# Kernel tuning notes

Measured on AMD Instinct MI355X. Metric: run time of the kernel, lower is better.

Reference implementation:

```python
import jax, jax.numpy as jnp
import numpy as np

D_IN = 1024
D_OUT = 1024
NUM_HEADS = 16
HEAD_DIM = D_OUT // NUM_HEADS


def setup_inputs() -> dict:
    key = jax.random.key(0)
    k_x, k_qkv, k_pw, k_pb = jax.random.split(key, 4)
    x = jax.random.normal(k_x, (2, 2048, D_IN), dtype=jnp.float32)
    # torch nn.Linear(d_in, 3*d_out, bias=False): weight [3*d_out, d_in]
    w_qkv = jax.random.normal(k_qkv, (3 * D_OUT, D_IN), dtype=jnp.float32) * (1.0 / np.sqrt(D_IN))
    # proj: nn.Linear(d_out, d_out) with bias
    w_proj = jax.random.normal(k_pw, (D_OUT, D_OUT), dtype=jnp.float32) * (1.0 / np.sqrt(D_OUT))
    b_proj = jax.random.normal(k_pb, (D_OUT,), dtype=jnp.float32) * 0.01
    return {"x": x, "w_qkv": w_qkv, "w_proj": w_proj, "b_proj": b_proj}


def reference(x, w_qkv, w_proj, b_proj):
    B, S, _ = x.shape
    # fused QKV projection: [B,S,3*D_OUT]
    qkv = jnp.einsum('bsd,ed->bse', x, w_qkv)
    qkv = qkv.reshape(B, S, 3, NUM_HEADS, HEAD_DIM)
    q, k, v = jnp.moveaxis(qkv, 2, 0)  # each [B,S,H,Dh]
    scale = 1.0 / jnp.sqrt(jnp.asarray(HEAD_DIM, dtype=x.dtype))
    # scores [B,H,S,S]
    scores = jnp.einsum('bqhd,bkhd->bhqk', q, k) * scale
    causal = jnp.tril(jnp.ones((S, S), dtype=bool))
    scores = jnp.where(causal, scores, jnp.asarray(-jnp.inf, dtype=scores.dtype))
    attn = jax.nn.softmax(scores, axis=-1)
    ctx = jnp.einsum('bhqk,bkhd->bqhd', attn, v)  # [B,S,H,Dh]
    ctx = ctx.reshape(B, S, D_OUT)
    return jnp.einsum('bsd,ed->bse', ctx, w_proj) + b_proj
```

## Files before the change

kernel.cpp:

```cpp
#include <hip/hip_runtime.h>
#include <hip/hip_bf16.h>
#include <cstdint>

#define B_SZ   2
#define S_LEN  2048
#define NH     16
#define NT     32
#define LDA    72

using f32x4 = __attribute__((ext_vector_type(4))) float;
typedef __bf16 bf16x8 __attribute__((ext_vector_type(8)));
typedef __bf16 bf16x4 __attribute__((ext_vector_type(4)));

__device__ inline float bf2f(unsigned short u) {
    union { unsigned int i; float f; } v; v.i = ((unsigned int)u) << 16; return v.f;
}
__device__ inline unsigned short f2bf(float f) {
    union { float f; unsigned int i; } v; v.f = f;
    unsigned int r = v.i + 0x7fff + ((v.i >> 16) & 1);
    return (unsigned short)(r >> 16);
}
__device__ inline f32x4 mfma16(bf16x8 a, bf16x8 b, f32x4 c) {
    return __builtin_amdgcn_mfma_f32_16x16x32_bf16(a, b, c, 0, 0, 0);
}
__device__ inline unsigned pack_bf16x2(float lo, float hi) {
    float2 f2; f2.x = lo; f2.y = hi;
    __hip_bfloat162 bb = __float22bfloat162_rn(f2);
    union { __hip_bfloat162 b; unsigned u; } cv; cv.b = bb;
    return cv.u;
}
__device__ inline void ldsbar() {
    __builtin_amdgcn_sched_barrier(0);
    asm volatile("s_waitcnt lgkmcnt(0)" ::: "memory");
    __builtin_amdgcn_s_barrier();
    __builtin_amdgcn_sched_barrier(0);
}
__device__ inline void stC(float* C, size_t idx, float v)  { C[idx] = v; }
__device__ inline void stC(__bf16* C, size_t idx, float v) { ((unsigned short*)C)[idx] = f2bf(v); }

__global__ __launch_bounds__(256) void f2b2_kernel(
    const float* __restrict__ a, int na4, __bf16* __restrict__ outa,
    const float* __restrict__ b, int nb4, __bf16* __restrict__ outb)
{
    int i = blockIdx.x * blockDim.x + threadIdx.x;
    const float* src; __bf16* dst; int idx;
    if (i < na4)           { src = a; dst = outa; idx = i; }
    else if (i < na4 + nb4){ src = b; dst = outb; idx = i - na4; }
    else return;
    float4 v = ((const float4*)src)[idx];
    ushort4 o;
    o.x = f2bf(v.x); o.y = f2bf(v.y); o.z = f2bf(v.z); o.w = f2bf(v.w);
    ((ushort4*)dst)[idx] = o;
}

__global__ __launch_bounds__(256) void f2b_kernel(
    const float* __restrict__ in, __bf16* __restrict__ out, int n4)
{
    int i = blockIdx.x * blockDim.x + threadIdx.x;
    if (i < n4) {
        float4 v = ((const float4*)in)[i];
        ushort4 o;
        o.x = f2bf(v.x); o.y = f2bf(v.y); o.z = f2bf(v.z); o.w = f2bf(v.w);
        ((ushort4*)out)[i] = o;
    }
}

template <typename TO, int HAS_BIAS>
__global__ __launch_bounds__(256) void gemm128(
    const __bf16* __restrict__ A, const __bf16* __restrict__ W,
    const float* __restrict__ bias, TO* __restrict__ C,
    int M, int N, int K)
{
    __shared__ __bf16 Alds[2][128 * 32];
    __shared__ __bf16 Blds[2][128 * 32];
    const int tid  = threadIdx.x, lane = tid & 63, w = tid >> 6;
    const int c16  = lane & 15, quad = lane >> 4;
    const int mBase = blockIdx.y * 128, nBase = blockIdx.x * 128;
    const int moff = (w & 1) * 64, noff = (w >> 1) * 64;

    f32x4 acc[4][4];
#pragma unroll
    for (int i = 0; i < 4; ++i)
#pragma unroll
        for (int j = 0; j < 4; ++j) acc[i][j] = (f32x4){0.f, 0.f, 0.f, 0.f};

    auto stage = [&](int buf, int k0) {
#pragma unroll
        for (int p = 0; p < 2; ++p) {
            const int linear = p * 256 + tid;
            const int row = linear >> 2;
            const int seg = (linear & 3) ^ (row & 3);
            const int lbase = (p * 256 + w * 64) * 8;
            const __bf16* ga = A + (size_t)(mBase + row) * K + k0 + seg * 8;
            const __bf16* gb = W + (size_t)(nBase + row) * K + k0 + seg * 8;
            __builtin_amdgcn_global_load_lds(
                (const __attribute__((address_space(1))) void*)ga,
                (__attribute__((address_space(3))) void*)(&Alds[buf][lbase]), 16, 0, 0);
            __builtin_amdgcn_global_load_lds(
                (const __attribute__((address_space(1))) void*)gb,
                (__attribute__((address_space(3))) void*)(&Blds[buf][lbase]), 16, 0, 0);
        }
    };

    stage(0, 0);
    int cur = 0;
    for (int k0 = 0; k0 < K; k0 += 32) {
        __syncthreads();
        if (k0 + 32 < K) stage(cur ^ 1, k0 + 32);

        bf16x8 af[4], bw[4];
#pragma unroll
        for (int i = 0; i < 4; ++i) {
            const int rowA = moff + i * 16 + c16;
            af[i] = *(const bf16x8*)&Alds[cur][rowA * 32 + ((quad ^ (rowA & 3)) << 3)];
            const int rowB = noff + i * 16 + c16;
            bw[i] = *(const bf16x8*)&Blds[cur][rowB * 32 + ((quad ^ (rowB & 3)) << 3)];
        }
#pragma unroll
        for (int i = 0; i < 4; ++i)
#pragma unroll
            for (int j = 0; j < 4; ++j)
                acc[i][j] = mfma16(af[i], bw[j], acc[i][j]);
        cur ^= 1;
    }

#pragma unroll
    for (int j = 0; j < 4; ++j) {
        const int col = nBase + noff + j * 16 + c16;
        const float bv = HAS_BIAS ? bias[col] : 0.f;
#pragma unroll
        for (int i = 0; i < 4; ++i)
#pragma unroll
            for (int r = 0; r < 4; ++r) {
                const int row = mBase + moff + i * 16 + quad * 4 + r;
                stC(C, (size_t)row * N + col, acc[i][j][r] + bv);
            }
    }
}

template <typename TO, int HAS_BIAS>
__global__ __launch_bounds__(256) void gemm64(
    const __bf16* __restrict__ A, const __bf16* __restrict__ W,
    const float* __restrict__ bias, TO* __restrict__ C,
    int M, int N, int K)
{
    __shared__ __bf16 Alds[2][64 * 32];
    __shared__ __bf16 Blds[2][128 * 32];
    const int tid  = threadIdx.x, lane = tid & 63, w = tid >> 6;
    const int c16  = lane & 15, quad = lane >> 4;
    const int mBase = blockIdx.y * 64, nBase = blockIdx.x * 128;
    const int moff = (w & 1) * 32, noff = (w >> 1) * 64;

    f32x4 acc[2][4];
#pragma unroll
    for (int i = 0; i < 2; ++i)
#pragma unroll
        for (int j = 0; j < 4; ++j) acc[i][j] = (f32x4){0.f, 0.f, 0.f, 0.f};

    auto stage = [&](int buf, int k0) {
        {
            const int row = tid >> 2;
            const int seg = (tid & 3) ^ (row & 3);
            const int lbase = (w * 64) * 8;
            const __bf16* ga = A + (size_t)(mBase + row) * K + k0 + seg * 8;
            __builtin_amdgcn_global_load_lds(
                (const __attribute__((address_space(1))) void*)ga,
                (__attribute__((address_space(3))) void*)(&Alds[buf][lbase]), 16, 0, 0);
        }
#pragma unroll
        for (int p = 0; p < 2; ++p) {
            const int linear = p * 256 + tid;
            const int row = linear >> 2;
            const int seg = (linear & 3) ^ (row & 3);
            const int lbase = (p * 256 + w * 64) * 8;
            const __bf16* gb = W + (size_t)(nBase + row) * K + k0 + seg * 8;
            __builtin_amdgcn_global_load_lds(
                (const __attribute__((address_space(1))) void*)gb,
                (__attribute__((address_space(3))) void*)(&Blds[buf][lbase]), 16, 0, 0);
        }
    };

    stage(0, 0);
    int cur = 0;
    for (int k0 = 0; k0 < K; k0 += 32) {
        __syncthreads();
        if (k0 + 32 < K) stage(cur ^ 1, k0 + 32);

        bf16x8 af[2], bw[4];
#pragma unroll
        for (int i = 0; i < 2; ++i) {
            const int rowA = moff + i * 16 + c16;
            af[i] = *(const bf16x8*)&Alds[cur][rowA * 32 + ((quad ^ (rowA & 3)) << 3)];
        }
#pragma unroll
        for (int j = 0; j < 4; ++j) {
            const int rowB = noff + j * 16 + c16;
            bw[j] = *(const bf16x8*)&Blds[cur][rowB * 32 + ((quad ^ (rowB & 3)) << 3)];
        }
#pragma unroll
        for (int i = 0; i < 2; ++i)
#pragma unroll
            for (int j = 0; j < 4; ++j)
                acc[i][j] = mfma16(af[i], bw[j], acc[i][j]);
        cur ^= 1;
    }

#pragma unroll
    for (int j = 0; j < 4; ++j) {
        const int col = nBase + noff + j * 16 + c16;
        const float bv = HAS_BIAS ? bias[col] : 0.f;
#pragma unroll
        for (int i = 0; i < 2; ++i)
#pragma unroll
            for (int r = 0; r < 4; ++r) {
                const int row = mBase + moff + i * 16 + quad * 4 + r;
                stC(C, (size_t)row * N + col, acc[i][j][r] + bv);
            }
    }
}

__global__ __launch_bounds__(256) void attn(
    const __bf16* __restrict__ qkv, __bf16* __restrict__ ctx,
    float* __restrict__ opart, float* __restrict__ lpart)
{
    __shared__ __bf16 Qs[64 * LDA];
    __shared__ __bf16 Ks[64 * LDA];
    __shared__ __bf16 Vs[64 * LDA];

    const int tid  = threadIdx.x;
    const int lane = tid & 63;
    const int w    = tid >> 6;
    const int c16  = lane & 15;
    const int quad = lane >> 4;
    const int bh = blockIdx.x, b = bh >> 4, h = bh & 15;
    const int y  = blockIdx.y;

    int qt, c0, c1, seg;
    bool split;
    if (y < 16)      { qt = 16 + y; const int half = (qt + 2) >> 1; c0 = 0;    c1 = half;   split = true;  seg = 0; }
    else if (y < 32) { qt = y;      const int half = (qt + 2) >> 1; c0 = half; c1 = qt + 1; split = true;  seg = 1; }
    else             { qt = 47 - y; c0 = 0; c1 = qt + 1; split = false; seg = 0; }
    const int qBase = qt * 64;
    const int segIdx = split ? ((bh * 16 + (qt - 16)) * 2 + seg) : 0;

    const float QS = 0.125f * 1.4426950408889634f;

    const int krow0 = tid >> 3;
    const int kd0   = (tid & 7) * 8;
    const int u     = tid & 31;
    const int dblk  = tid >> 5;
    const int vcol  = 32 * (u & 1) + 8 * ((u >> 1) & 3) + 2 * (u >> 3);

    const size_t rowB = (size_t)b * S_LEN;
    const __bf16* kp0 = qkv + (rowB + c0 * 64 + krow0) * 3072 + 1024 + h * 64 + kd0;
    const __bf16* kp1 = kp0 + (size_t)32 * 3072;
    const __bf16* vp0 = qkv + (rowB + c0 * 64 + 2 * u) * 3072 + 2048 + h * 64 + dblk * 8;
    const __bf16* vp1 = vp0 + (size_t)3072;

    uint4 kr0 = *(const uint4*)kp0;
    uint4 kr1 = *(const uint4*)kp1;
    uint4 vr0 = *(const uint4*)vp0;
    uint4 vr1 = *(const uint4*)vp1;

#pragma unroll
    for (int p = 0; p < 2; ++p) {
        const int linear = p * 256 + tid;
        const int row = linear >> 3;
        const int d0 = (linear & 7) * 8;
        const __bf16* g = qkv + (rowB + qBase + row) * 3072 + h * 64 + d0;
        uint4 raw = *(const uint4*)g;
        const unsigned short* uu = (const unsigned short*)&raw;
        unsigned short tmp[8];
#pragma unroll
        for (int jj = 0; jj < 8; ++jj) tmp[jj] = f2bf(bf2f(uu[jj]) * QS);
        *(uint4*)&Qs[row * LDA + d0] = *(const uint4*)tmp;
    }
    ldsbar();

    const bf16x8 aq0 = *(const bf16x8*)&Qs[(w * 16 + c16) * LDA + quad * 8];
    const bf16x8 aq1 = *(const bf16x8*)&Qs[(w * 16 + c16) * LDA + 32 + quad * 8];

    float lp = 0.f;
    f32x4 acc_o[4];
#pragma unroll
    for (int j = 0; j < 4; ++j) acc_o[j] = (f32x4){0.f, 0.f, 0.f, 0.f};

    for (int cc = c0; cc < c1; ++cc) {
        *(uint4*)&Ks[krow0 * LDA + kd0]        = kr0;
        *(uint4*)&Ks[(krow0 + 32) * LDA + kd0] = kr1;
        {
            const unsigned short* e1 = (const unsigned short*)&vr0;
            const unsigned short* e2 = (const unsigned short*)&vr1;
#pragma unroll
            for (int d = 0; d < 8; ++d) {
                const unsigned pack = (unsigned)e1[d] | ((unsigned)e2[d] << 16);
                *(unsigned*)&Vs[(dblk * 8 + d) * LDA + vcol] = pack;
            }
        }
        ldsbar();

        if (cc + 1 < c1) {
            kp0 += (size_t)64 * 3072; kp1 += (size_t)64 * 3072;
            vp0 += (size_t)64 * 3072; vp1 += (size_t)64 * 3072;
            kr0 = *(const uint4*)kp0;
            kr1 = *(const uint4*)kp1;
            vr0 = *(const uint4*)vp0;
            vr1 = *(const uint4*)vp1;
        }

        f32x4 sc[4];
#pragma unroll
        for (int j = 0; j < 4; ++j) sc[j] = (f32x4){0.f, 0.f, 0.f, 0.f};
#pragma unroll
        for (int j = 0; j < 4; ++j) {
            bf16x8 bk0 = *(const bf16x8*)&Ks[(j * 16 + c16) * LDA + quad * 8];
            bf16x8 bk1 = *(const bf16x8*)&Ks[(j * 16 + c16) * LDA + 32 + quad * 8];
            sc[j] = mfma16(bk0, aq0, sc[j]);
            sc[j] = mfma16(bk1, aq1, sc[j]);
        }

        if (cc == qt) {
            const int q = qBase + w * 16 + c16;
#pragma unroll
            for (int j = 0; j < 4; ++j) {
#pragma unroll
                for (int r = 0; r < 4; ++r) {
                    const int key = cc * 64 + j * 16 + quad * 4 + r;
                    if (key > q) sc[j][r] = -1e30f;
                }
            }
        }

        float p_[4][4];
#pragma unroll
        for (int j = 0; j < 4; ++j)
#pragma unroll
            for (int r = 0; r < 4; ++r)
                p_[j][r] = exp2f(sc[j][r]);
#pragma unroll
        for (int j = 0; j < 4; ++j)
            lp += (p_[j][0] + p_[j][1]) + (p_[j][2] + p_[j][3]);

        union { unsigned uu[4]; bf16x8 v; } B0, B1;
#pragma unroll
        for (int j = 0; j < 4; ++j) {
            B0.uu[j] = pack_bf16x2(p_[j][0], p_[j][1]);
            B1.uu[j] = pack_bf16x2(p_[j][2], p_[j][3]);
        }
        const bf16x8 bp0 = B0.v;
        const bf16x8 bp1 = B1.v;

#pragma unroll
        for (int jd = 0; jd < 4; ++jd) {
            bf16x8 av0 = *(const bf16x8*)&Vs[(jd * 16 + c16) * LDA + quad * 8];
            bf16x8 av1 = *(const bf16x8*)&Vs[(jd * 16 + c16) * LDA + 32 + quad * 8];
            acc_o[jd] = mfma16(av0, bp0, acc_o[jd]);
            acc_o[jd] = mfma16(av1, bp1, acc_o[jd]);
        }
        ldsbar();
    }

    lp += __shfl_xor(lp, 16);
    lp += __shfl_xor(lp, 32);

    if (!split) {
        const float inv = 1.0f / lp;
        const size_t rowO = (rowB + qBase + w * 16 + c16) * 1024 + h * 64;
#pragma unroll
        for (int jd = 0; jd < 4; ++jd) {
            bf16x4 ov;
#pragma unroll
            for (int r = 0; r < 4; ++r) ov[r] = (__bf16)(acc_o[jd][r] * inv);
            *(bf16x4*)&ctx[rowO + jd * 16 + quad * 4] = ov;
        }
    } else {
        float* ob = opart + (size_t)segIdx * 4096 + (w * 16 + c16) * 64;
        if (quad == 0) lpart[segIdx * 64 + w * 16 + c16] = lp;
#pragma unroll
        for (int jd = 0; jd < 4; ++jd)
            *(f32x4*)&ob[jd * 16 + quad * 4] = acc_o[jd];
    }
}

__global__ __launch_bounds__(256) void attn_combine(
    const float* __restrict__ opart, const float* __restrict__ lpart,
    __bf16* __restrict__ ctx)
{
    const int blk = blockIdx.x;
    const int bh = blk >> 4, t = blk & 15;
    const int b = bh >> 4, h = bh & 15;
    const int qt = 16 + t;
    const int tid = threadIdx.x;
    const int q  = tid >> 2;
    const int d0 = (tid & 3) * 16;
    const int segA = blk * 2, segB = segA + 1;
    const float* oa = opart + (size_t)segA * 4096 + q * 64 + d0;
    const float* obp = opart + (size_t)segB * 4096 + q * 64 + d0;
    const float inv = 1.0f / (lpart[segA * 64 + q] + lpart[segB * 64 + q]);
    unsigned short outv[16];
#pragma unroll
    for (int i = 0; i < 4; ++i) {
        float4 a = ((const float4*)oa)[i];
        float4 c = ((const float4*)obp)[i];
        outv[4 * i + 0] = f2bf((a.x + c.x) * inv);
        outv[4 * i + 1] = f2bf((a.y + c.y) * inv);
        outv[4 * i + 2] = f2bf((a.z + c.z) * inv);
        outv[4 * i + 3] = f2bf((a.w + c.w) * inv);
    }
    __bf16* dst = ctx + ((size_t)(b * S_LEN + qt * 64 + q)) * 1024 + h * 64 + d0;
    *(uint4*)dst       = *(const uint4*)&outv[0];
    *(uint4*)(dst + 8) = *(const uint4*)&outv[8];
}

extern "C" void kernel_launch(void* const* d_in, const int* in_sizes, int n_in,
                              void* d_out, int out_size, void* d_ws, size_t ws_size,
                              hipStream_t stream) {
    const float* x      = (const float*)d_in[0];
    const float* w_qkv  = (const float*)d_in[1];
    const float* w_proj = (const float*)d_in[2];
    const float* b_proj = (const float*)d_in[3];
    float* out = (float*)d_out;

    __bf16* qkvb = (__bf16*)d_ws;
    __bf16* xb   = qkvb + (size_t)4096 * 3072;
    __bf16* wqb  = xb + (size_t)4096 * 1024;
    __bf16* ctxb = xb;
    __bf16* wpb  = wqb;
    float*  lpart = (float*)(wqb + (size_t)1024 * 1024);
    float* opart = out;

    const int M = B_SZ * S_LEN;
    const int nx4 = 4096 * 1024 / 4, nq4 = 3072 * 1024 / 4, np4 = 1024 * 1024 / 4;

    f2b2_kernel<<<(nx4 + nq4 + 255) / 256, 256, 0, stream>>>(x, nx4, xb, w_qkv, nq4, wqb);

    gemm128<__bf16, 0><<<dim3(3072 / 128, M / 128), 256, 0, stream>>>(
        xb, wqb, nullptr, qkvb, M, 3072, 1024);

    f2b_kernel<<<(np4 + 255) / 256, 256, 0, stream>>>(w_proj, wpb, np4);

    attn<<<dim3(B_SZ * NH, 48), 256, 0, stream>>>(qkvb, ctxb, opart, lpart);
    attn_combine<<<B_SZ * NH * 16, 256, 0, stream>>>(opart, lpart, ctxb);

    gemm64<float, 1><<<dim3(1024 / 128, M / 64), 256, 0, stream>>>(
        ctxb, wpb, b_proj, out, M, 1024, 1024);
}
```

Measured before the change: 185.2 us.

## Pair causal query tiles per block instead of split-KV with combine kernel

Attention work is rebalanced by giving each block two query tiles, a long one (16+y) and a short one (15-y), processed one after the other, so every block does the same total number of key tiles. This removes the split-KV partial outputs, the global fp32 partial buffers and the separate combine kernel launch. In exchange the grid shrinks from 1536 to 512 blocks, which lowers parallelism and latency hiding across the GPU's compute units, and each block runs two serial passes.

```diff
diff --git a/kernel.cpp b/kernel.cpp
--- a/kernel.cpp
+++ b/kernel.cpp
@@ -220,8 +220,7 @@
 }
 
 __global__ __launch_bounds__(256) void attn(
-    const __bf16* __restrict__ qkv, __bf16* __restrict__ ctx,
-    float* __restrict__ opart, float* __restrict__ lpart)
+    const __bf16* __restrict__ qkv, __bf16* __restrict__ ctx)
 {
     __shared__ __bf16 Qs[64 * LDA];
     __shared__ __bf16 Ks[64 * LDA];
@@ -235,14 +234,6 @@
     const int bh = blockIdx.x, b = bh >> 4, h = bh & 15;
     const int y  = blockIdx.y;
 
-    int qt, c0, c1, seg;
-    bool split;
-    if (y < 16)      { qt = 16 + y; const int half = (qt + 2) >> 1; c0 = 0;    c1 = half;   split = true;  seg = 0; }
-    else if (y < 32) { qt = y;      const int half = (qt + 2) >> 1; c0 = half; c1 = qt + 1; split = true;  seg = 1; }
-    else             { qt = 47 - y; c0 = 0; c1 = qt + 1; split = false; seg = 0; }
-    const int qBase = qt * 64;
-    const int segIdx = split ? ((bh * 16 + (qt - 16)) * 2 + seg) : 0;
-
     const float QS = 0.125f * 1.4426950408889634f;
 
     const int krow0 = tid >> 3;
@@ -252,118 +243,123 @@
     const int vcol  = 32 * (u & 1) + 8 * ((u >> 1) & 3) + 2 * (u >> 3);
 
     const size_t rowB = (size_t)b * S_LEN;
-    const __bf16* kp0 = qkv + (rowB + c0 * 64 + krow0) * 3072 + 1024 + h * 64 + kd0;
-    const __bf16* kp1 = kp0 + (size_t)32 * 3072;
-    const __bf16* vp0 = qkv + (rowB + c0 * 64 + 2 * u) * 3072 + 2048 + h * 64 + dblk * 8;
-    const __bf16* vp1 = vp0 + (size_t)3072;
-
-    uint4 kr0 = *(const uint4*)kp0;
-    uint4 kr1 = *(const uint4*)kp1;
-    uint4 vr0 = *(const uint4*)vp0;
-    uint4 vr1 = *(const uint4*)vp1;
-
-#pragma unroll
-    for (int p = 0; p < 2; ++p) {
-        const int linear = p * 256 + tid;
-        const int row = linear >> 3;
-        const int d0 = (linear & 7) * 8;
-        const __bf16* g = qkv + (rowB + qBase + row) * 3072 + h * 64 + d0;
-        uint4 raw = *(const uint4*)g;
-        const unsigned short* uu = (const unsigned short*)&raw;
-        unsigned short tmp[8];
-#pragma unroll
-        for (int jj = 0; jj < 8; ++jj) tmp[jj] = f2bf(bf2f(uu[jj]) * QS);
-        *(uint4*)&Qs[row * LDA + d0] = *(const uint4*)tmp;
-    }
-    ldsbar();
-
-    const bf16x8 aq0 = *(const bf16x8*)&Qs[(w * 16 + c16) * LDA + quad * 8];
-    const bf16x8 aq1 = *(const bf16x8*)&Qs[(w * 16 + c16) * LDA + 32 + quad * 8];
-
-    float lp = 0.f;
-    f32x4 acc_o[4];
-#pragma unroll
-    for (int j = 0; j < 4; ++j) acc_o[j] = (f32x4){0.f, 0.f, 0.f, 0.f};
-
-    for (int cc = c0; cc < c1; ++cc) {
-        *(uint4*)&Ks[krow0 * LDA + kd0]        = kr0;
-        *(uint4*)&Ks[(krow0 + 32) * LDA + kd0] = kr1;
-        {
-            const unsigned short* e1 = (const unsigned short*)&vr0;
-            const unsigned short* e2 = (const unsigned short*)&vr1;
-#pragma unroll
-            for (int d = 0; d < 8; ++d) {
-                const unsigned pack = (unsigned)e1[d] | ((unsigned)e2[d] << 16);
-                *(unsigned*)&Vs[(dblk * 8 + d) * LDA + vcol] = pack;
-            }
+
+    for (int tt = 0; tt < 2; ++tt) {
+        const int qt = (tt == 0) ? (16 + y) : (15 - y);
+        const int c1 = qt + 1;
+        const int qBase = qt * 64;
+
+        const __bf16* kp0 = qkv + (rowB + krow0) * 3072 + 1024 + h * 64 + kd0;
+        const __bf16* kp1 = kp0 + (size_t)32 * 3072;
+        const __bf16* vp0 = qkv + (rowB + 2 * u) * 3072 + 2048 + h * 64 + dblk * 8;
+        const __bf16* vp1 = vp0 + (size_t)3072;
+
+        uint4 kr0 = *(const uint4*)kp0;
+        uint4 kr1 = *(const uint4*)kp1;
+        uint4 vr0 = *(const uint4*)vp0;
+        uint4 vr1 = *(const uint4*)vp1;
+
+#pragma unroll
+        for (int p = 0; p < 2; ++p) {
+            const int linear = p * 256 + tid;
+            const int row = linear >> 3;
+            const int d0 = (linear & 7) * 8;
+            const __bf16* g = qkv + (rowB + qBase + row) * 3072 + h * 64 + d0;
+            uint4 raw = *(const uint4*)g;
+            const unsigned short* uu = (const unsigned short*)&raw;
+            unsigned short tmp[8];
+#pragma unroll
+            for (int jj = 0; jj < 8; ++jj) tmp[jj] = f2bf(bf2f(uu[jj]) * QS);
+            *(uint4*)&Qs[row * LDA + d0] = *(const uint4*)tmp;
         }
         ldsbar();
 
-        if (cc + 1 < c1) {
-            kp0 += (size_t)64 * 3072; kp1 += (size_t)64 * 3072;
-            vp0 += (size_t)64 * 3072; vp1 += (size_t)64 * 3072;
-            kr0 = *(const uint4*)kp0;
-            kr1 = *(const uint4*)kp1;
-            vr0 = *(const uint4*)vp0;
-            vr1 = *(const uint4*)vp1;
-        }
-
-        f32x4 sc[4];
-#pragma unroll
-        for (int j = 0; j < 4; ++j) sc[j] = (f32x4){0.f, 0.f, 0.f, 0.f};
-#pragma unroll
-        for (int j = 0; j < 4; ++j) {
-            bf16x8 bk0 = *(const bf16x8*)&Ks[(j * 16 + c16) * LDA + quad * 8];
-            bf16x8 bk1 = *(const bf16x8*)&Ks[(j * 16 + c16) * LDA + 32 + quad * 8];
-            sc[j] = mfma16(bk0, aq0, sc[j]);
-            sc[j] = mfma16(bk1, aq1, sc[j]);
-        }
-
-        if (cc == qt) {
-            const int q = qBase + w * 16 + c16;
+        const bf16x8 aq0 = *(const bf16x8*)&Qs[(w * 16 + c16) * LDA + quad * 8];
+        const bf16x8 aq1 = *(const bf16x8*)&Qs[(w * 16 + c16) * LDA + 32 + quad * 8];
+
+        float lp = 0.f;
+        f32x4 acc_o[4];
+#pragma unroll
+        for (int j = 0; j < 4; ++j) acc_o[j] = (f32x4){0.f, 0.f, 0.f, 0.f};
+
+        for (int cc = 0; cc < c1; ++cc) {
+            *(uint4*)&Ks[krow0 * LDA + kd0]        = kr0;
+            *(uint4*)&Ks[(krow0 + 32) * LDA + kd0] = kr1;
+            {
+                const unsigned short* e1 = (const unsigned short*)&vr0;
+                const unsigned short* e2 = (const unsigned short*)&vr1;
+#pragma unroll
+                for (int d = 0; d < 8; ++d) {
+                    const unsigned pack = (unsigned)e1[d] | ((unsigned)e2[d] << 16);
+                    *(unsigned*)&Vs[(dblk * 8 + d) * LDA + vcol] = pack;
+                }
+            }
+            ldsbar();
+
+            if (cc + 1 < c1) {
+                kp0 += (size_t)64 * 3072; kp1 += (size_t)64 * 3072;
+                vp0 += (size_t)64 * 3072; vp1 += (size_t)64 * 3072;
+                kr0 = *(const uint4*)kp0;
+                kr1 = *(const uint4*)kp1;
+                vr0 = *(const uint4*)vp0;
+                vr1 = *(const uint4*)vp1;
+            }
+
+            f32x4 sc[4];
+#pragma unroll
+            for (int j = 0; j < 4; ++j) sc[j] = (f32x4){0.f, 0.f, 0.f, 0.f};
 #pragma unroll
             for (int j = 0; j < 4; ++j) {
-#pragma unroll
-                for (int r = 0; r < 4; ++r) {
-                    const int key = cc * 64 + j * 16 + quad * 4 + r;
-                    if (key > q) sc[j][r] = -1e30f;
+                bf16x8 bk0 = *(const bf16x8*)&Ks[(j * 16 + c16) * LDA + quad * 8];
+                bf16x8 bk1 = *(const bf16x8*)&Ks[(j * 16 + c16) * LDA + 32 + quad * 8];
+                sc[j] = mfma16(bk0, aq0, sc[j]);
+                sc[j] = mfma16(bk1, aq1, sc[j]);
+            }
+
+            if (cc == qt) {
+                const int q = qBase + w * 16 + c16;
+#pragma unroll
+                for (int j = 0; j < 4; ++j) {
+#pragma unroll
+                    for (int r = 0; r < 4; ++r) {
+                        const int key = cc * 64 + j * 16 + quad * 4 + r;
+                        if (key > q) sc[j][r] = -1e30f;
+                    }
                 }
             }
-        }
-
-        float p_[4][4];
-#pragma unroll
-        for (int j = 0; j < 4; ++j)
-#pragma unroll
-            for (int r = 0; r < 4; ++r)
-                p_[j][r] = exp2f(sc[j][r]);
-#pragma unroll
-        for (int j = 0; j < 4; ++j)
-            lp += (p_[j][0] + p_[j][1]) + (p_[j][2] + p_[j][3]);
-
-        union { unsigned uu[4]; bf16x8 v; } B0, B1;
-#pragma unroll
-        for (int j = 0; j < 4; ++j) {
-            B0.uu[j] = pack_bf16x2(p_[j][0], p_[j][1]);
-            B1.uu[j] = pack_bf16x2(p_[j][2], p_[j][3]);
-        }
-        const bf16x8 bp0 = B0.v;
-        const bf16x8 bp1 = B1.v;
-
-#pragma unroll
-        for (int jd = 0; jd < 4; ++jd) {
-            bf16x8 av0 = *(const bf16x8*)&Vs[(jd * 16 + c16) * LDA + quad * 8];
-            bf16x8 av1 = *(const bf16x8*)&Vs[(jd * 16 + c16) * LDA + 32 + quad * 8];
-            acc_o[jd] = mfma16(av0, bp0, acc_o[jd]);
-            acc_o[jd] = mfma16(av1, bp1, acc_o[jd]);
-        }
-        ldsbar();
-    }
-
-    lp += __shfl_xor(lp, 16);
-    lp += __shfl_xor(lp, 32);
-
-    if (!split) {
+
+            float p_[4][4];
+#pragma unroll
+            for (int j = 0; j < 4; ++j)
+#pragma unroll
+                for (int r = 0; r < 4; ++r)
+                    p_[j][r] = exp2f(sc[j][r]);
+#pragma unroll
+            for (int j = 0; j < 4; ++j)
+                lp += (p_[j][0] + p_[j][1]) + (p_[j][2] + p_[j][3]);
+
+            union { unsigned uu[4]; bf16x8 v; } B0, B1;
+#pragma unroll
+            for (int j = 0; j < 4; ++j) {
+                B0.uu[j] = pack_bf16x2(p_[j][0], p_[j][1]);
+                B1.uu[j] = pack_bf16x2(p_[j][2], p_[j][3]);
+            }
+            const bf16x8 bp0 = B0.v;
+            const bf16x8 bp1 = B1.v;
+
+#pragma unroll
+            for (int jd = 0; jd < 4; ++jd) {
+                bf16x8 av0 = *(const bf16x8*)&Vs[(jd * 16 + c16) * LDA + quad * 8];
+                bf16x8 av1 = *(const bf16x8*)&Vs[(jd * 16 + c16) * LDA + 32 + quad * 8];
+                acc_o[jd] = mfma16(av0, bp0, acc_o[jd]);
+                acc_o[jd] = mfma16(av1, bp1, acc_o[jd]);
+            }
+            ldsbar();
+        }
+
+        lp += __shfl_xor(lp, 16);
+        lp += __shfl_xor(lp, 32);
+
         const float inv = 1.0f / lp;
         const size_t rowO = (rowB + qBase + w * 16 + c16) * 1024 + h * 64;
 #pragma unroll
@@ -373,43 +369,7 @@
             for (int r = 0; r < 4; ++r) ov[r] = (__bf16)(acc_o[jd][r] * inv);
             *(bf16x4*)&ctx[rowO + jd * 16 + quad * 4] = ov;
         }
-    } else {
-        float* ob = opart + (size_t)segIdx * 4096 + (w * 16 + c16) * 64;
-        if (quad == 0) lpart[segIdx * 64 + w * 16 + c16] = lp;
-#pragma unroll
-        for (int jd = 0; jd < 4; ++jd)
-            *(f32x4*)&ob[jd * 16 + quad * 4] = acc_o[jd];
-    }
-}
-
-__global__ __launch_bounds__(256) void attn_combine(
-    const float* __restrict__ opart, const float* __restrict__ lpart,
-    __bf16* __restrict__ ctx)
-{
-    const int blk = blockIdx.x;
-    const int bh = blk >> 4, t = blk & 15;
-    const int b = bh >> 4, h = bh & 15;
-    const int qt = 16 + t;
-    const int tid = threadIdx.x;
-    const int q  = tid >> 2;
-    const int d0 = (tid & 3) * 16;
-    const int segA = blk * 2, segB = segA + 1;
-    const float* oa = opart + (size_t)segA * 4096 + q * 64 + d0;
-    const float* obp = opart + (size_t)segB * 4096 + q * 64 + d0;
-    const float inv = 1.0f / (lpart[segA * 64 + q] + lpart[segB * 64 + q]);
-    unsigned short outv[16];
-#pragma unroll
-    for (int i = 0; i < 4; ++i) {
-        float4 a = ((const float4*)oa)[i];
-        float4 c = ((const float4*)obp)[i];
-        outv[4 * i + 0] = f2bf((a.x + c.x) * inv);
-        outv[4 * i + 1] = f2bf((a.y + c.y) * inv);
-        outv[4 * i + 2] = f2bf((a.z + c.z) * inv);
-        outv[4 * i + 3] = f2bf((a.w + c.w) * inv);
-    }
-    __bf16* dst = ctx + ((size_t)(b * S_LEN + qt * 64 + q)) * 1024 + h * 64 + d0;
-    *(uint4*)dst       = *(const uint4*)&outv[0];
-    *(uint4*)(dst + 8) = *(const uint4*)&outv[8];
+    }
 }
 
 extern "C" void kernel_launch(void* const* d_in, const int* in_sizes, int n_in,
@@ -426,8 +386,6 @@
     __bf16* wqb  = xb + (size_t)4096 * 1024;
     __bf16* ctxb = xb;
     __bf16* wpb  = wqb;
-    float*  lpart = (float*)(wqb + (size_t)1024 * 1024);
-    float* opart = out;
 
     const int M = B_SZ * S_LEN;
     const int nx4 = 4096 * 1024 / 4, nq4 = 3072 * 1024 / 4, np4 = 1024 * 1024 / 4;
@@ -439,8 +397,7 @@
 
     f2b_kernel<<<(np4 + 255) / 256, 256, 0, stream>>>(w_proj, wpb, np4);
 
-    attn<<<dim3(B_SZ * NH, 48), 256, 0, stream>>>(qkvb, ctxb, opart, lpart);
-    attn_combine<<<B_SZ * NH * 16, 256, 0, stream>>>(opart, lpart, ctxb);
+    attn<<<dim3(B_SZ * NH, 16), 256, 0, stream>>>(qkvb, ctxb);
 
     gemm64<float, 1><<<dim3(1024 / 128, M / 64), 256, 0, stream>>>(
         ctxb, wpb, b_proj, out, M, 1024, 1024);
```

New measurement: 192.6 us. +4.0%, slower.
